# Kernel optimization log

Measured on AMD Instinct MI355X. Metric: run time of the kernel, lower is better.

The kernel has to match this reference:

```python
import jax, jax.numpy as jnp
import numpy as np

N, E, R, F, HD = 4096, 2048, 4, 128, 256
DEG_EPS = 1e-8
BN_EPS = 1e-5
LN_EPS = 1e-5


def _xavier(k, shape):
    scale = np.sqrt(2.0 / (shape[-2] + shape[-1])).astype(np.float32)
    return jax.random.normal(k, shape, jnp.float32) * scale


def setup_inputs() -> dict:
    key = jax.random.key(0)
    ks = jax.random.split(key, 8)
    X = jax.random.normal(ks[0], (N, F), jnp.float32)
    # sparse binary incidence matrices, one per relation type, stacked [R,N,E]
    H = (jax.random.uniform(ks[1], (R, N, E)) < 0.05).astype(jnp.float32)
    return {
        "X": X,
        "H": H,
        "W1": _xavier(ks[2], (R, F, HD)),
        "W2": _xavier(ks[3], (R, HD, HD)),
        "W3": _xavier(ks[4], (R, HD, F)),
        "imp": jnp.ones((3, R), jnp.float32),        # relation_importance per conv layer
        "b1": jnp.zeros((HD,), jnp.float32),
        "b2": jnp.zeros((HD,), jnp.float32),
        "b3": jnp.zeros((F,), jnp.float32),
        "bn_gamma": jnp.ones((2, HD), jnp.float32),
        "bn_beta": jnp.zeros((2, HD), jnp.float32),
        "ln_gamma": jnp.ones((2, HD), jnp.float32),
        "ln_beta": jnp.zeros((2, HD), jnp.float32),
        "rel_attn": jnp.ones((R,), jnp.float32) / R,
    }


def typed_conv(X, Hw, W, imp, bias):
    # Hw: [R,N,E] weighted incidence; theta = Dv^{-1/2} H De^{-1/2} via row/col scaling
    dv = jnp.power(Hw.sum(axis=2) + DEG_EPS, -0.5)   # [R,N]
    de = jnp.power(Hw.sum(axis=1) + DEG_EPS, -0.5)   # [R,E]
    theta = Hw * dv[:, :, None] * de[:, None, :]     # [R,N,E]
    # (theta @ theta^T) @ X computed as theta @ (theta^T @ X) -- same math, no NxN
    t = jnp.einsum('rne,nf->ref', theta, X)          # [R,E,Fin]
    Hn = jnp.einsum('rne,ref->rnf', theta, t)        # [R,N,Fin]
    out = jnp.einsum('rnf,rfo->rno', Hn, W)          # [R,N,Fout]
    out = out * jax.nn.sigmoid(imp)[:, None, None]
    return out.sum(axis=0) + bias


def bn_ln_elu(X, bg, bb, lg, lb):
    # BatchNorm1d with batch statistics (biased var), then LayerNorm, then ELU
    mu = X.mean(axis=0)
    var = X.var(axis=0)
    X = (X - mu) * jax.lax.rsqrt(var + BN_EPS) * bg + bb
    m = X.mean(axis=-1, keepdims=True)
    v = X.var(axis=-1, keepdims=True)
    X = (X - m) * jax.lax.rsqrt(v + LN_EPS) * lg + lb
    return jax.nn.elu(X)


def reference(X, H, W1, W2, W3, imp, b1, b2, b3, bn_gamma, bn_beta, ln_gamma, ln_beta, rel_attn):
    rw = jax.nn.softmax(rel_attn)
    Hw = H * rw[:, None, None]                       # weighted incidence per relation
    h = typed_conv(X, Hw, W1, imp[0], b1)
    h = bn_ln_elu(h, bn_gamma[0], bn_beta[0], ln_gamma[0], ln_beta[0])
    h = typed_conv(h, Hw, W2, imp[1], b2)
    h = bn_ln_elu(h, bn_gamma[1], bn_beta[1], ln_gamma[1], ln_beta[1])
    out = typed_conv(h, Hw, W3, imp[2], b3)
    return out + X  # residual: out_channels == in_channels by construction
```

## Files before the change

kernel.cpp:

```cpp
#include <hip/hip_runtime.h>
#include <hip/hip_bf16.h>

#define NN 4096
#define EE 2048
#define RR 4
#define FF 128
#define HDD 256

typedef __attribute__((ext_vector_type(4))) float floatx4;
typedef __attribute__((ext_vector_type(8))) __bf16 bf16x8;

#define AS1 __attribute__((address_space(1)))
#define AS3 __attribute__((address_space(3)))

__device__ __forceinline__ void async16(const void* g, void* l) {
  __builtin_amdgcn_global_load_lds((const AS1 void*)(unsigned long long)(g),
                                   (AS3 void*)(unsigned int)(unsigned long long)(l),
                                   16, 0, 0);
}

__device__ inline unsigned short f2b(float x) {
  unsigned int u = __float_as_uint(x);
  unsigned int r = u + 0x7fffu + ((u >> 16) & 1u);
  return (unsigned short)(r >> 16);
}
__device__ inline float b2f(unsigned short u) { return __uint_as_float((unsigned int)u << 16); }

__device__ inline float rel_w(const float* rel, int r) {
  float m = fmaxf(fmaxf(rel[0], rel[1]), fmaxf(rel[2], rel[3]));
  float s = 0.f;
#pragma unroll
  for (int i = 0; i < RR; i++) s += expf(rel[i] - m);
  return expf(rel[r] - m) / s;
}

__global__ void k_dvmask(const float* __restrict__ H, const float* __restrict__ rel,
                         float* __restrict__ dvs, unsigned long long* __restrict__ mask) {
  int wave = (blockIdx.x << 2) | (threadIdx.x >> 6);
  int lane = threadIdx.x & 63;
  int r = wave >> 12;
  const float* row = H + (size_t)wave * EE;
  unsigned long long* mrow = mask + (size_t)wave * (EE / 64);
  float s = 0.f;
  for (int j = 0; j < EE / 64; j++) {
    float h = row[j * 64 + lane];
    s += h;
    unsigned long long m = __ballot(h != 0.0f);
    if (lane == 0) mrow[j] = m;
  }
  for (int off = 32; off; off >>= 1) s += __shfl_down(s, off);
  if (lane == 0) {
    float rwr = rel_w(rel, r);
    dvs[wave] = rwr * rsqrtf(rwr * s + 1e-8f);
  }
}

__global__ void k_maskT(const unsigned long long* __restrict__ m1, unsigned long long* __restrict__ m2,
                        float* __restrict__ de) {
  __shared__ unsigned long long w[64 * 33];
  int r = blockIdx.x >> 6;
  int n0 = (blockIdx.x & 63) << 6;
  int t = threadIdx.x;
  const unsigned long long* src = m1 + ((size_t)r * NN + n0) * 32;
#pragma unroll
  for (int i = 0; i < 8; i++) {
    int idx = t + i * 256;
    int n = idx >> 5, W = idx & 31;
    w[n * 33 + W] = src[idx];
  }
  __syncthreads();
  int wid = t >> 6, lane = t & 63;
  int v = n0 >> 6;
#pragma unroll
  for (int Wi = 0; Wi < 8; Wi++) {
    int W = wid * 8 + Wi;
    unsigned long long myw = w[lane * 33 + W];
    unsigned long long out = 0;
    for (int b = 0; b < 64; b++) {
      unsigned long long mm = __ballot(((myw >> b) & 1ULL) != 0);
      if (lane == b) out = mm;
    }
    m2[((size_t)r * EE + W * 64 + lane) * 64 + v] = out;
    atomicAdd(&de[r * EE + W * 64 + lane], (float)__popcll(out));
  }
}

__global__ void k_deR(const float* __restrict__ de, const float* __restrict__ rel,
                      float* __restrict__ deR, float* __restrict__ deR2) {
  int i = blockIdx.x * 256 + threadIdx.x;
  int r = i >> 11;
  float rwr = rel_w(rel, r);
  float d = rsqrtf(rwr * de[i] + 1e-8f);
  deR[i] = d;
  deR2[i] = d * d;
}

__global__ void k_cvtTs(const float* __restrict__ src, const float* __restrict__ dvs,
                        unsigned short* __restrict__ dst, int M, int C) {
  __shared__ unsigned short tile[64][65];
  int r = blockIdx.z;
  int c0 = blockIdx.x * 64, m0 = blockIdx.y * 64;
  int tr = threadIdx.x >> 4, tc = threadIdx.x & 15;
#pragma unroll
  for (int i = 0; i < 4; i++) {
    int m = m0 + tr + 16 * i;
    float d = dvs[(size_t)r * M + m];
    float4 v = *(const float4*)(src + (size_t)m * C + c0 + tc * 4);
    tile[tr + 16 * i][tc * 4 + 0] = f2b(v.x * d);
    tile[tr + 16 * i][tc * 4 + 1] = f2b(v.y * d);
    tile[tr + 16 * i][tc * 4 + 2] = f2b(v.z * d);
    tile[tr + 16 * i][tc * 4 + 3] = f2b(v.w * d);
  }
  __syncthreads();
  unsigned short* db = dst + (size_t)r * C * M;
#pragma unroll
  for (int i = 0; i < 4; i++) {
    int c = c0 + tr + 16 * i;
    ushort4 v;
    v.x = tile[tc * 4 + 0][tr + 16 * i];
    v.y = tile[tc * 4 + 1][tr + 16 * i];
    v.z = tile[tc * 4 + 2][tr + 16 * i];
    v.w = tile[tc * 4 + 3][tr + 16 * i];
    *(ushort4*)(db + (size_t)c * M + m0 + tc * 4) = v;
  }
}

__global__ void k_trzs(const unsigned short* __restrict__ src, const float* __restrict__ dvs,
                       unsigned short* __restrict__ dst, int M, int C) {
  __shared__ unsigned short tile[64][65];
  int r = blockIdx.z;
  int c0 = blockIdx.x * 64, m0 = blockIdx.y * 64;
  int tr = threadIdx.x >> 4, tc = threadIdx.x & 15;
#pragma unroll
  for (int i = 0; i < 4; i++) {
    int m = m0 + tr + 16 * i;
    float d = dvs[(size_t)r * M + m];
    ushort4 v = *(const ushort4*)(src + (size_t)m * C + c0 + tc * 4);
    tile[tr + 16 * i][tc * 4 + 0] = f2b(b2f(v.x) * d);
    tile[tr + 16 * i][tc * 4 + 1] = f2b(b2f(v.y) * d);
    tile[tr + 16 * i][tc * 4 + 2] = f2b(b2f(v.z) * d);
    tile[tr + 16 * i][tc * 4 + 3] = f2b(b2f(v.w) * d);
  }
  __syncthreads();
  unsigned short* db = dst + (size_t)r * C * M;
#pragma unroll
  for (int i = 0; i < 4; i++) {
    int c = c0 + tr + 16 * i;
    ushort4 v;
    v.x = tile[tc * 4 + 0][tr + 16 * i];
    v.y = tile[tc * 4 + 1][tr + 16 * i];
    v.z = tile[tc * 4 + 2][tr + 16 * i];
    v.w = tile[tc * 4 + 3][tr + 16 * i];
    *(ushort4*)(db + (size_t)c * M + m0 + tc * 4) = v;
  }
}

__global__ void k_wprep(const float* __restrict__ W1, const float* __restrict__ W2,
                        const float* __restrict__ W3, const float* __restrict__ imp,
                        unsigned short* __restrict__ W1catT, unsigned short* __restrict__ W2T,
                        unsigned short* __restrict__ W3T) {
  int idx = blockIdx.x * 256 + threadIdx.x;
  if (idx < RR * FF * HDD) {
    int o = idx % HDD, f = (idx / HDD) % FF, r = idx / (HDD * FF);
    float sg = 1.0f / (1.0f + expf(-imp[r]));
    W1catT[(size_t)o * (RR * FF) + r * FF + f] = f2b(sg * W1[((size_t)r * FF + f) * HDD + o]);
  } else if (idx < RR * FF * HDD + RR * HDD * HDD) {
    int j = idx - RR * FF * HDD;
    int c = j % HDD, o = (j / HDD) % HDD, r = j / (HDD * HDD);
    float sg = 1.0f / (1.0f + expf(-imp[RR + r]));
    W2T[j] = f2b(sg * W2[((size_t)r * HDD + c) * HDD + o]);
  } else {
    int j = idx - RR * FF * HDD - RR * HDD * HDD;
    int c = j % HDD, o = (j / HDD) % FF, r = j / (HDD * FF);
    float sg = 1.0f / (1.0f + expf(-imp[2 * RR + r]));
    W3T[j] = f2b(sg * W3[((size_t)r * HDD + c) * FF + o]);
  }
}

template <int DECA, int DECB>
__global__ __launch_bounds__(256) void k_gemm3(
    const unsigned short* __restrict__ A, const unsigned short* __restrict__ BT,
    int K, int SK, int lda, int ldb, long a_rs, long b_rs,
    unsigned short* __restrict__ P, long c_ps, long c_rs, int ldc,
    const unsigned long long* __restrict__ dm, int dnw, long drow_rs,
    const float* __restrict__ cscale, long cs_rs) {
  __shared__ unsigned short Al[128 * 64];
  __shared__ unsigned short Bl[128 * 64];
  int tid = threadIdx.x, wid = tid >> 6, lane = tid & 63;
  int m0 = blockIdx.x << 7, n0 = blockIdx.y << 7;
  int z = blockIdx.z, zr = z / SK, kz = z - zr * SK;
  int Kc = K / SK;
  int r8 = lane >> 3, c8 = lane & 7;
  int swz = ((c8 ^ r8) << 3);
  const unsigned short* Ab = A + (DECA ? 0 : ((size_t)zr * a_rs + (size_t)m0 * lda + (size_t)kz * Kc));
  const unsigned short* Bb = BT + (DECB ? 0 : ((size_t)zr * b_rs + (size_t)n0 * ldb + (size_t)kz * Kc));
  const unsigned int* mrow = nullptr;
  int drow = 0, dhalf = 0, dsw = 0;
  unsigned short* Dl = DECA ? Al : Bl;
  if (DECA || DECB) {
    drow = tid >> 1; dhalf = tid & 1;
    long mrowOff = (long)zr * drow_rs + (DECA ? m0 : n0) + drow;
    mrow = (const unsigned int*)(dm + (size_t)mrowOff * dnw);
    dsw = drow & 7;
  }
  int wm = (wid >> 1) << 6, wn = (wid & 1) << 6;
  int fm = lane & 15, quad = lane >> 4;
  int f7 = fm & 7;
  floatx4 acc[4][4];
#pragma unroll
  for (int i = 0; i < 4; i++)
#pragma unroll
    for (int j = 0; j < 4; j++) acc[i][j] = (floatx4){0.f, 0.f, 0.f, 0.f};
  for (int k0 = 0; k0 < Kc; k0 += 64) {
    if (!DECA) {
#pragma unroll
      for (int t = 0; t < 4; t++) {
        int rbase = (wid << 5) + (t << 3);
        int row = rbase + r8;
        async16(Ab + (size_t)row * lda + k0 + swz, &Al[rbase * 64 + lane * 8]);
      }
    }
    if (!DECB) {
#pragma unroll
      for (int t = 0; t < 4; t++) {
        int rbase = (wid << 5) + (t << 3);
        int row = rbase + r8;
        async16(Bb + (size_t)row * ldb + k0 + swz, &Bl[rbase * 64 + lane * 8]);
      }
    }
    if (DECA || DECB) {
      long kglob = (long)kz * Kc + k0;
      unsigned int bits = mrow[(kglob >> 5) + dhalf];
      uint4 zz = {0u, 0u, 0u, 0u};
#pragma unroll
      for (int g = 0; g < 4; g++) {
        int chunk = ((dhalf << 2) | g) ^ dsw;
        *(uint4*)&Dl[drow * 64 + chunk * 8] = zz;
      }
      while (bits) {
        int b = __builtin_ctz(bits);
        bits &= bits - 1;
        int kl = (dhalf << 5) + b;
        Dl[drow * 64 + (((kl >> 3) ^ dsw) << 3) + (kl & 7)] = (unsigned short)0x3F80;
      }
    }
    __syncthreads();
#pragma unroll
    for (int ks = 0; ks < 2; ks++) {
      int kg = (ks << 2) | quad;
      int ko = ((kg ^ f7) << 3);
      bf16x8 a[4], b[4];
#pragma unroll
      for (int i = 0; i < 4; i++) {
        a[i] = *(const bf16x8*)&Al[(wm + i * 16 + fm) * 64 + ko];
        b[i] = *(const bf16x8*)&Bl[(wn + i * 16 + fm) * 64 + ko];
      }
#pragma unroll
      for (int i = 0; i < 4; i++)
#pragma unroll
        for (int j = 0; j < 4; j++)
          acc[i][j] = __builtin_amdgcn_mfma_f32_16x16x32_bf16(a[i], b[j], acc[i][j], 0, 0, 0);
    }
    __syncthreads();
  }
  unsigned short* Cb = P + (size_t)kz * c_ps + (size_t)zr * c_rs;
  float csc[4];
#pragma unroll
  for (int ni = 0; ni < 4; ni++)
    csc[ni] = cscale ? cscale[(size_t)zr * cs_rs + n0 + wn + ni * 16 + fm] : 1.0f;
#pragma unroll
  for (int mi = 0; mi < 4; mi++)
#pragma unroll
    for (int ni = 0; ni < 4; ni++)
#pragma unroll
      for (int v = 0; v < 4; v++) {
        int row = m0 + wm + mi * 16 + quad * 4 + v;
        int col = n0 + wn + ni * 16 + fm;
        Cb[(size_t)row * ldc + col] = f2b(acc[mi][ni][v] * csc[ni]);
      }
}

__global__ void k_red_b(const unsigned short* __restrict__ P, unsigned short* __restrict__ out,
                        int SK, long region,
                        const float* __restrict__ sc, long sc_rs, int sc_shift, int sc_mask) {
  long i = ((long)blockIdx.x * 256 + threadIdx.x) * 8;
  int zr = blockIdx.y;
  const unsigned short* p = P + (size_t)zr * SK * region + i;
  float s[8] = {0, 0, 0, 0, 0, 0, 0, 0};
  for (int k = 0; k < SK; k++) {
    const unsigned short* q = p + (size_t)k * region;
    ushort4 a = *(const ushort4*)q;
    ushort4 b = *(const ushort4*)(q + 4);
    s[0] += b2f(a.x); s[1] += b2f(a.y); s[2] += b2f(a.z); s[3] += b2f(a.w);
    s[4] += b2f(b.x); s[5] += b2f(b.y); s[6] += b2f(b.z); s[7] += b2f(b.w);
  }
  float scl[8];
#pragma unroll
  for (int j = 0; j < 8; j++)
    scl[j] = sc ? sc[(size_t)zr * sc_rs + (int)(((i + j) >> sc_shift) & sc_mask)] : 1.0f;
  ushort4 o0, o1;
  o0.x = f2b(s[0] * scl[0]); o0.y = f2b(s[1] * scl[1]); o0.z = f2b(s[2] * scl[2]); o0.w = f2b(s[3] * scl[3]);
  o1.x = f2b(s[4] * scl[4]); o1.y = f2b(s[5] * scl[5]); o1.z = f2b(s[6] * scl[6]); o1.w = f2b(s[7] * scl[7]);
  unsigned short* d = out + (size_t)zr * region + i;
  *(ushort4*)d = o0;
  *(ushort4*)(d + 4) = o1;
}

__global__ void k_red_hcatb(const unsigned short* __restrict__ P, unsigned short* __restrict__ out,
                            int SK, const float* __restrict__ dvs) {
  long i = ((long)blockIdx.x * 256 + threadIdx.x) * 8;
  int r = blockIdx.y;
  const unsigned short* p = P + (size_t)r * SK * (NN * FF) + i;
  float s[8] = {0, 0, 0, 0, 0, 0, 0, 0};
  for (int k = 0; k < SK; k++) {
    const unsigned short* q = p + (size_t)k * (NN * FF);
    ushort4 a = *(const ushort4*)q;
    ushort4 b = *(const ushort4*)(q + 4);
    s[0] += b2f(a.x); s[1] += b2f(a.y); s[2] += b2f(a.z); s[3] += b2f(a.w);
    s[4] += b2f(b.x); s[5] += b2f(b.y); s[6] += b2f(b.z); s[7] += b2f(b.w);
  }
  long n = i >> 7;
  int f = (int)(i & 127);
  float dv = dvs[(size_t)r * NN + n];
  ushort4 o0, o1;
  o0.x = f2b(s[0] * dv); o0.y = f2b(s[1] * dv); o0.z = f2b(s[2] * dv); o0.w = f2b(s[3] * dv);
  o1.x = f2b(s[4] * dv); o1.y = f2b(s[5] * dv); o1.z = f2b(s[6] * dv); o1.w = f2b(s[7] * dv);
  unsigned short* d = out + n * (RR * FF) + r * FF + f;
  *(ushort4*)d = o0;
  *(ushort4*)(d + 4) = o1;
}

__global__ void k_redstats(const unsigned short* __restrict__ P, float* __restrict__ out,
                           float* __restrict__ cs, float* __restrict__ cs2, int Z,
                           const float* __restrict__ rs, int rshift) {
  __shared__ float sm[2][8][256];
  int cg = (threadIdx.x & 31) << 3;
  int rowt = threadIdx.x >> 5;
  int r0 = blockIdx.x * 32;
  float s[8] = {0, 0, 0, 0, 0, 0, 0, 0}, s2[8] = {0, 0, 0, 0, 0, 0, 0, 0};
  for (int j = 0; j < 4; j++) {
    int row = r0 + rowt * 4 + j;
    long idx = (long)row * HDD + cg;
    float acc[8] = {0, 0, 0, 0, 0, 0, 0, 0};
    for (int z = 0; z < Z; z++) {
      const unsigned short* p = P + (size_t)z * ((long)NN * HDD) + idx;
      float w_ = rs ? rs[(size_t)(z >> rshift) * NN + row] : 1.0f;
      ushort4 a = *(const ushort4*)p;
      ushort4 b = *(const ushort4*)(p + 4);
      acc[0] += b2f(a.x) * w_; acc[1] += b2f(a.y) * w_; acc[2] += b2f(a.z) * w_; acc[3] += b2f(a.w) * w_;
      acc[4] += b2f(b.x) * w_; acc[5] += b2f(b.y) * w_; acc[6] += b2f(b.z) * w_; acc[7] += b2f(b.w) * w_;
    }
    float4 o0 = {acc[0], acc[1], acc[2], acc[3]};
    float4 o1 = {acc[4], acc[5], acc[6], acc[7]};
    *(float4*)(out + idx) = o0;
    *(float4*)(out + idx + 4) = o1;
#pragma unroll
    for (int i = 0; i < 8; i++) { s[i] += acc[i]; s2[i] += acc[i] * acc[i]; }
  }
#pragma unroll
  for (int i = 0; i < 8; i++) { sm[0][rowt][cg + i] = s[i]; sm[1][rowt][cg + i] = s2[i]; }
  __syncthreads();
  int c = threadIdx.x;
  float a0 = 0, a1 = 0;
#pragma unroll
  for (int t = 0; t < 8; t++) { a0 += sm[0][t][c]; a1 += sm[1][t][c]; }
  atomicAdd(&cs[c], a0);
  atomicAdd(&cs2[c], a1);
}

__global__ void k_red_out(const unsigned short* __restrict__ P, const float* __restrict__ X,
                          const float* __restrict__ b3, float* __restrict__ out, int Z,
                          const float* __restrict__ rs) {
  long i = ((long)blockIdx.x * 256 + threadIdx.x) * 4;
  long n = i >> 7;
  int f = (int)(i & 127);
  float4 s = *(const float4*)(X + i);
  s.x += b3[f]; s.y += b3[f + 1]; s.z += b3[f + 2]; s.w += b3[f + 3];
  for (int z = 0; z < Z; z++) {
    float w_ = rs[(size_t)(z >> 1) * NN + n];
    ushort4 v = *(const ushort4*)(P + (size_t)z * (NN * FF) + i);
    s.x += b2f(v.x) * w_; s.y += b2f(v.y) * w_; s.z += b2f(v.z) * w_; s.w += b2f(v.w) * w_;
  }
  *(float4*)(out + i) = s;
}

__global__ void k_bnlnelu(const float* __restrict__ x, const float* __restrict__ cs, const float* __restrict__ cs2,
                          const float* __restrict__ bg, const float* __restrict__ bb,
                          const float* __restrict__ lg, const float* __restrict__ lb,
                          unsigned short* __restrict__ out) {
  int wid = threadIdx.x >> 6, lane = threadIdx.x & 63;
  int n = blockIdx.x * 4 + wid;
  float y[4];
  float m = 0.f;
#pragma unroll
  for (int j = 0; j < 4; j++) {
    int c = lane + 64 * j;
    float mu = cs[c] * (1.0f / NN);
    float var = cs2[c] * (1.0f / NN) - mu * mu;
    float xv = x[(size_t)n * HDD + c];
    y[j] = (xv - mu) * rsqrtf(var + 1e-5f) * bg[c] + bb[c];
    m += y[j];
  }
  for (int off = 32; off; off >>= 1) m += __shfl_down(m, off);
  m = __shfl(m, 0) * (1.0f / HDD);
  float var = 0.f;
#pragma unroll
  for (int j = 0; j < 4; j++) { float d = y[j] - m; var += d * d; }
  for (int off = 32; off; off >>= 1) var += __shfl_down(var, off);
  var = __shfl(var, 0) * (1.0f / HDD);
  float inv = rsqrtf(var + 1e-5f);
#pragma unroll
  for (int j = 0; j < 4; j++) {
    int c = lane + 64 * j;
    float z = (y[j] - m) * inv * lg[c] + lb[c];
    z = z > 0.f ? z : expm1f(z);
    out[(size_t)n * HDD + c] = f2b(z);
  }
}

extern "C" void kernel_launch(void* const* d_in, const int* in_sizes, int n_in,
                              void* d_out, int out_size, void* d_ws, size_t ws_size,
                              hipStream_t stream) {
  const float* X   = (const float*)d_in[0];
  const float* H   = (const float*)d_in[1];
  const float* W1  = (const float*)d_in[2];
  const float* W2  = (const float*)d_in[3];
  const float* W3  = (const float*)d_in[4];
  const float* imp = (const float*)d_in[5];
  const float* b3  = (const float*)d_in[8];
  const float* bng = (const float*)d_in[9];
  const float* bnb = (const float*)d_in[10];
  const float* lng = (const float*)d_in[11];
  const float* lnb = (const float*)d_in[12];
  const float* rel = (const float*)d_in[13];
  (void)in_sizes; (void)n_in; (void)out_size; (void)ws_size;

  char* w = (char*)d_ws;
  size_t off = 0;
  auto alloc = [&](size_t bytes) -> void* {
    void* p = w + off;
    off += (bytes + 255) & ~(size_t)255;
    return p;
  };
  float* dvs  = (float*)alloc((size_t)RR * NN * 4);
  float* de   = (float*)alloc((size_t)RR * EE * 4);
  float* deR  = (float*)alloc((size_t)RR * EE * 4);
  float* deR2 = (float*)alloc((size_t)RR * EE * 4);
  float* cs   = (float*)alloc(2 * HDD * 4);
  unsigned long long* mask1 = (unsigned long long*)alloc((size_t)RR * NN * (EE / 64) * 8);
  unsigned long long* mask2 = (unsigned long long*)alloc((size_t)RR * EE * (NN / 64) * 8);
  unsigned short* bufP = (unsigned short*)alloc((size_t)16 * NN * HDD * 2);
  unsigned short* bufC = (unsigned short*)alloc((size_t)RR * EE * HDD * 2);
  unsigned short* bufD = (unsigned short*)alloc((size_t)RR * EE * HDD * 2);
  unsigned short* bufE = (unsigned short*)alloc((size_t)RR * EE * HDD * 2);
  float* convout = (float*)alloc((size_t)NN * HDD * 4);
  unsigned short* Xb   = (unsigned short*)alloc((size_t)NN * HDD * 2);
  unsigned short* XdvT = (unsigned short*)alloc((size_t)RR * FF * NN * 2);
  unsigned short* hdvT = (unsigned short*)alloc((size_t)RR * HDD * NN * 2);
  unsigned short* W1catT = (unsigned short*)alloc((size_t)RR * FF * HDD * 2);
  unsigned short* W2T    = (unsigned short*)alloc((size_t)RR * HDD * HDD * 2);
  unsigned short* W3T    = (unsigned short*)alloc((size_t)RR * HDD * FF * 2);

  k_dvmask<<<(RR * NN) / 4, 256, 0, stream>>>(H, rel, dvs, mask1);
  hipMemsetAsync(de, 0, (size_t)RR * EE * 4, stream);
  k_maskT<<<RR * (NN / 64), 256, 0, stream>>>(mask1, mask2, de);
  k_deR<<<(RR * EE) / 256, 256, 0, stream>>>(de, rel, deR, deR2);
  k_cvtTs<<<dim3(FF / 64, NN / 64, RR), 256, 0, stream>>>(X, dvs, XdvT, NN, FF);
  k_wprep<<<(RR * FF * HDD + RR * HDD * HDD + RR * HDD * FF) / 256, 256, 0, stream>>>(
      W1, W2, W3, imp, W1catT, W2T, W3T);

  k_gemm3<0, 1><<<dim3(1, EE / 128, RR * 8), 256, 0, stream>>>(
      XdvT, nullptr, NN, 8, NN, 0, (long)FF * NN, 0,
      bufP, (long)FF * EE, 8L * FF * EE, EE, mask2, NN / 64, EE, nullptr, 0);
  k_red_b<<<dim3((FF * EE) / 2048, RR), 256, 0, stream>>>(
      bufP, bufC, 8, (long)FF * EE, deR2, EE, 0, EE - 1);
  k_gemm3<1, 0><<<dim3(NN / 128, 1, RR * 2), 256, 0, stream>>>(
      nullptr, bufC, EE, 2, 0, EE, 0, (long)FF * EE,
      bufP, (long)NN * FF, 2L * NN * FF, FF, mask1, EE / 64, NN, nullptr, 0);
  k_red_hcatb<<<dim3((NN * FF) / 2048, RR), 256, 0, stream>>>(bufP, bufD, 2, dvs);
  k_gemm3<0, 0><<<dim3(NN / 128, HDD / 128, 4), 256, 0, stream>>>(
      bufD, W1catT, RR * FF, 4, RR * FF, RR * FF, 0, 0,
      bufP, (long)NN * HDD, 0, HDD, nullptr, 0, 0, nullptr, 0);
  hipMemsetAsync(cs, 0, 2 * HDD * 4, stream);
  k_redstats<<<NN / 32, 256, 0, stream>>>(bufP, convout, cs, cs + HDD, 4, nullptr, 0);
  k_bnlnelu<<<NN / 4, 256, 0, stream>>>(convout, cs, cs + HDD, bng, bnb, lng, lnb, Xb);
  k_trzs<<<dim3(HDD / 64, NN / 64, RR), 256, 0, stream>>>(Xb, dvs, hdvT, NN, HDD);

  k_gemm3<1, 0><<<dim3(EE / 128, HDD / 128, RR * 4), 256, 0, stream>>>(
      nullptr, hdvT, NN, 4, 0, NN, 0, (long)HDD * NN,
      bufP, (long)RR * EE * HDD, (long)EE * HDD, HDD, mask2, NN / 64, EE, nullptr, 0);
  k_red_b<<<dim3((RR * EE * HDD) / 2048, 1), 256, 0, stream>>>(
      bufP, bufD, 4, (long)RR * EE * HDD, deR, 0, 8, RR * EE - 1);
  k_gemm3<0, 0><<<dim3(HDD / 128, EE / 128, RR), 256, 0, stream>>>(
      W2T, bufD, HDD, 1, HDD, HDD, (long)HDD * HDD, (long)EE * HDD,
      bufE, 0, (long)HDD * EE, EE, nullptr, 0, 0, deR, EE);
  k_gemm3<1, 0><<<dim3(NN / 128, HDD / 128, RR * 2), 256, 0, stream>>>(
      nullptr, bufE, EE, 2, 0, EE, 0, (long)HDD * EE,
      bufP, (long)NN * HDD, 2L * NN * HDD, HDD, mask1, EE / 64, NN, nullptr, 0);
  hipMemsetAsync(cs, 0, 2 * HDD * 4, stream);
  k_redstats<<<NN / 32, 256, 0, stream>>>(bufP, convout, cs, cs + HDD, 8, dvs, 1);
  k_bnlnelu<<<NN / 4, 256, 0, stream>>>(convout, cs, cs + HDD, bng + HDD, bnb + HDD, lng + HDD, lnb + HDD, Xb);

  k_gemm3<0, 0><<<dim3(1, NN / 128, RR), 256, 0, stream>>>(
      W3T, Xb, HDD, 1, HDD, HDD, (long)FF * HDD, 0,
      bufD, 0, (long)FF * NN, NN, nullptr, 0, 0, dvs, NN);
  k_gemm3<0, 1><<<dim3(1, EE / 128, RR * 8), 256, 0, stream>>>(
      bufD, nullptr, NN, 8, NN, 0, (long)FF * NN, 0,
      bufP, (long)FF * EE, 8L * FF * EE, EE, mask2, NN / 64, EE, nullptr, 0);
  k_red_b<<<dim3((FF * EE) / 2048, RR), 256, 0, stream>>>(
      bufP, bufC, 8, (long)FF * EE, deR2, EE, 0, EE - 1);
  k_gemm3<1, 0><<<dim3(NN / 128, 1, RR * 2), 256, 0, stream>>>(
      nullptr, bufC, EE, 2, 0, EE, 0, (long)FF * EE,
      bufP, (long)NN * FF, 2L * NN * FF, FF, mask1, EE / 64, NN, nullptr, 0);
  k_red_out<<<(NN * FF) / 1024, 256, 0, stream>>>(bufP, X, b3, (float*)d_out, 8, dvs);
}
```

Baseline: 491.4 us.

## Fuse prep kernels, double-buffer GEMM LDS, and reorder layer-2 weight multiply

Merges the degree/mask, weight-prep and memset work into two combined prep kernels, and folds the de-scaling computation into the reduction kernel. This removes several small launches and memsets. The GEMM now double-buffers its LDS tiles so the next K-slice loads while the current one is computed. Layer 2 applies W2 before the hypergraph propagation (h·W then theta·theta^T), changing the GEMM chain and intermediate layouts. The costs are double the LDS per block, which may lower occupancy, a different bf16 rounding order in layer 2, and a K loop that assumes Kc is a multiple of 64.

```diff
diff --git a/kernel.cpp b/kernel.cpp
--- a/kernel.cpp
+++ b/kernel.cpp
@@ -34,146 +34,112 @@
   return expf(rel[r] - m) / s;
 }
 
-__global__ void k_dvmask(const float* __restrict__ H, const float* __restrict__ rel,
-                         float* __restrict__ dvs, unsigned long long* __restrict__ mask) {
-  int wave = (blockIdx.x << 2) | (threadIdx.x >> 6);
-  int lane = threadIdx.x & 63;
-  int r = wave >> 12;
-  const float* row = H + (size_t)wave * EE;
-  unsigned long long* mrow = mask + (size_t)wave * (EE / 64);
-  float s = 0.f;
-  for (int j = 0; j < EE / 64; j++) {
-    float h = row[j * 64 + lane];
-    s += h;
-    unsigned long long m = __ballot(h != 0.0f);
-    if (lane == 0) mrow[j] = m;
-  }
-  for (int off = 32; off; off >>= 1) s += __shfl_down(s, off);
-  if (lane == 0) {
-    float rwr = rel_w(rel, r);
-    dvs[wave] = rwr * rsqrtf(rwr * s + 1e-8f);
-  }
-}
-
-__global__ void k_maskT(const unsigned long long* __restrict__ m1, unsigned long long* __restrict__ m2,
-                        float* __restrict__ de) {
+__global__ void k_prep1(const float* __restrict__ H, const float* __restrict__ rel,
+                        const float* __restrict__ W1, const float* __restrict__ W2,
+                        const float* __restrict__ W3, const float* __restrict__ imp,
+                        float* __restrict__ dvs, unsigned long long* __restrict__ mask,
+                        unsigned short* __restrict__ W1catT, unsigned short* __restrict__ W2T,
+                        unsigned short* __restrict__ W3T, float* __restrict__ de, float* __restrict__ cs) {
+  int b = blockIdx.x;
+  if (b < 4096) {
+    int wave = (b << 2) | (threadIdx.x >> 6);
+    int lane = threadIdx.x & 63;
+    int r = wave >> 12;
+    const float* row = H + (size_t)wave * EE;
+    unsigned long long* mrow = mask + (size_t)wave * (EE / 64);
+    float s = 0.f;
+    for (int j = 0; j < EE / 64; j++) {
+      float h = row[j * 64 + lane];
+      s += h;
+      unsigned long long m = __ballot(h != 0.0f);
+      if (lane == 0) mrow[j] = m;
+    }
+    for (int off = 32; off; off >>= 1) s += __shfl_down(s, off);
+    if (lane == 0) {
+      float rwr = rel_w(rel, r);
+      dvs[wave] = rwr * rsqrtf(rwr * s + 1e-8f);
+    }
+  } else if (b < 4096 + 2048) {
+    int idx = (b - 4096) * 256 + threadIdx.x;
+    if (idx < RR * FF * HDD) {
+      int o = idx % HDD, f = (idx / HDD) % FF, r = idx / (HDD * FF);
+      float sg = 1.0f / (1.0f + expf(-imp[r]));
+      W1catT[(size_t)o * (RR * FF) + r * FF + f] = f2b(sg * W1[((size_t)r * FF + f) * HDD + o]);
+    } else if (idx < RR * FF * HDD + RR * HDD * HDD) {
+      int j = idx - RR * FF * HDD;
+      int c = j % HDD, o = (j / HDD) % HDD, r = j / (HDD * HDD);
+      float sg = 1.0f / (1.0f + expf(-imp[RR + r]));
+      W2T[j] = f2b(sg * W2[((size_t)r * HDD + c) * HDD + o]);
+    } else {
+      int j = idx - RR * FF * HDD - RR * HDD * HDD;
+      int c = j % HDD, o = (j / HDD) % FF, r = j / (HDD * FF);
+      float sg = 1.0f / (1.0f + expf(-imp[2 * RR + r]));
+      W3T[j] = f2b(sg * W3[((size_t)r * HDD + c) * FF + o]);
+    }
+  } else {
+    int i = (b - 6144) * 256 + threadIdx.x;
+    if (i < RR * EE) de[i] = 0.f;
+    else if (i < RR * EE + 2 * HDD) cs[i - RR * EE] = 0.f;
+  }
+}
+
+__global__ void k_prep2(const unsigned long long* __restrict__ m1, unsigned long long* __restrict__ m2,
+                        float* __restrict__ de, const float* __restrict__ X,
+                        const float* __restrict__ dvs, unsigned short* __restrict__ XdvT) {
   __shared__ unsigned long long w[64 * 33];
-  int r = blockIdx.x >> 6;
-  int n0 = (blockIdx.x & 63) << 6;
+  __shared__ unsigned short tile[64][65];
   int t = threadIdx.x;
-  const unsigned long long* src = m1 + ((size_t)r * NN + n0) * 32;
-#pragma unroll
-  for (int i = 0; i < 8; i++) {
-    int idx = t + i * 256;
-    int n = idx >> 5, W = idx & 31;
-    w[n * 33 + W] = src[idx];
-  }
-  __syncthreads();
-  int wid = t >> 6, lane = t & 63;
-  int v = n0 >> 6;
-#pragma unroll
-  for (int Wi = 0; Wi < 8; Wi++) {
-    int W = wid * 8 + Wi;
-    unsigned long long myw = w[lane * 33 + W];
-    unsigned long long out = 0;
-    for (int b = 0; b < 64; b++) {
-      unsigned long long mm = __ballot(((myw >> b) & 1ULL) != 0);
-      if (lane == b) out = mm;
-    }
-    m2[((size_t)r * EE + W * 64 + lane) * 64 + v] = out;
-    atomicAdd(&de[r * EE + W * 64 + lane], (float)__popcll(out));
-  }
-}
-
-__global__ void k_deR(const float* __restrict__ de, const float* __restrict__ rel,
-                      float* __restrict__ deR, float* __restrict__ deR2) {
-  int i = blockIdx.x * 256 + threadIdx.x;
-  int r = i >> 11;
-  float rwr = rel_w(rel, r);
-  float d = rsqrtf(rwr * de[i] + 1e-8f);
-  deR[i] = d;
-  deR2[i] = d * d;
-}
-
-__global__ void k_cvtTs(const float* __restrict__ src, const float* __restrict__ dvs,
-                        unsigned short* __restrict__ dst, int M, int C) {
-  __shared__ unsigned short tile[64][65];
-  int r = blockIdx.z;
-  int c0 = blockIdx.x * 64, m0 = blockIdx.y * 64;
-  int tr = threadIdx.x >> 4, tc = threadIdx.x & 15;
-#pragma unroll
-  for (int i = 0; i < 4; i++) {
-    int m = m0 + tr + 16 * i;
-    float d = dvs[(size_t)r * M + m];
-    float4 v = *(const float4*)(src + (size_t)m * C + c0 + tc * 4);
-    tile[tr + 16 * i][tc * 4 + 0] = f2b(v.x * d);
-    tile[tr + 16 * i][tc * 4 + 1] = f2b(v.y * d);
-    tile[tr + 16 * i][tc * 4 + 2] = f2b(v.z * d);
-    tile[tr + 16 * i][tc * 4 + 3] = f2b(v.w * d);
-  }
-  __syncthreads();
-  unsigned short* db = dst + (size_t)r * C * M;
-#pragma unroll
-  for (int i = 0; i < 4; i++) {
-    int c = c0 + tr + 16 * i;
-    ushort4 v;
-    v.x = tile[tc * 4 + 0][tr + 16 * i];
-    v.y = tile[tc * 4 + 1][tr + 16 * i];
-    v.z = tile[tc * 4 + 2][tr + 16 * i];
-    v.w = tile[tc * 4 + 3][tr + 16 * i];
-    *(ushort4*)(db + (size_t)c * M + m0 + tc * 4) = v;
-  }
-}
-
-__global__ void k_trzs(const unsigned short* __restrict__ src, const float* __restrict__ dvs,
-                       unsigned short* __restrict__ dst, int M, int C) {
-  __shared__ unsigned short tile[64][65];
-  int r = blockIdx.z;
-  int c0 = blockIdx.x * 64, m0 = blockIdx.y * 64;
-  int tr = threadIdx.x >> 4, tc = threadIdx.x & 15;
-#pragma unroll
-  for (int i = 0; i < 4; i++) {
-    int m = m0 + tr + 16 * i;
-    float d = dvs[(size_t)r * M + m];
-    ushort4 v = *(const ushort4*)(src + (size_t)m * C + c0 + tc * 4);
-    tile[tr + 16 * i][tc * 4 + 0] = f2b(b2f(v.x) * d);
-    tile[tr + 16 * i][tc * 4 + 1] = f2b(b2f(v.y) * d);
-    tile[tr + 16 * i][tc * 4 + 2] = f2b(b2f(v.z) * d);
-    tile[tr + 16 * i][tc * 4 + 3] = f2b(b2f(v.w) * d);
-  }
-  __syncthreads();
-  unsigned short* db = dst + (size_t)r * C * M;
-#pragma unroll
-  for (int i = 0; i < 4; i++) {
-    int c = c0 + tr + 16 * i;
-    ushort4 v;
-    v.x = tile[tc * 4 + 0][tr + 16 * i];
-    v.y = tile[tc * 4 + 1][tr + 16 * i];
-    v.z = tile[tc * 4 + 2][tr + 16 * i];
-    v.w = tile[tc * 4 + 3][tr + 16 * i];
-    *(ushort4*)(db + (size_t)c * M + m0 + tc * 4) = v;
-  }
-}
-
-__global__ void k_wprep(const float* __restrict__ W1, const float* __restrict__ W2,
-                        const float* __restrict__ W3, const float* __restrict__ imp,
-                        unsigned short* __restrict__ W1catT, unsigned short* __restrict__ W2T,
-                        unsigned short* __restrict__ W3T) {
-  int idx = blockIdx.x * 256 + threadIdx.x;
-  if (idx < RR * FF * HDD) {
-    int o = idx % HDD, f = (idx / HDD) % FF, r = idx / (HDD * FF);
-    float sg = 1.0f / (1.0f + expf(-imp[r]));
-    W1catT[(size_t)o * (RR * FF) + r * FF + f] = f2b(sg * W1[((size_t)r * FF + f) * HDD + o]);
-  } else if (idx < RR * FF * HDD + RR * HDD * HDD) {
-    int j = idx - RR * FF * HDD;
-    int c = j % HDD, o = (j / HDD) % HDD, r = j / (HDD * HDD);
-    float sg = 1.0f / (1.0f + expf(-imp[RR + r]));
-    W2T[j] = f2b(sg * W2[((size_t)r * HDD + c) * HDD + o]);
+  if (blockIdx.x < 256) {
+    int r = blockIdx.x >> 6;
+    int n0 = (blockIdx.x & 63) << 6;
+    const unsigned long long* src = m1 + ((size_t)r * NN + n0) * 32;
+#pragma unroll
+    for (int i = 0; i < 8; i++) {
+      int idx = t + i * 256;
+      int n = idx >> 5, W = idx & 31;
+      w[n * 33 + W] = src[idx];
+    }
+    __syncthreads();
+    int wid = t >> 6, lane = t & 63;
+    int v = n0 >> 6;
+#pragma unroll
+    for (int Wi = 0; Wi < 8; Wi++) {
+      int W = wid * 8 + Wi;
+      unsigned long long myw = w[lane * 33 + W];
+      unsigned long long out = 0;
+      for (int b = 0; b < 64; b++) {
+        unsigned long long mm = __ballot(((myw >> b) & 1ULL) != 0);
+        if (lane == b) out = mm;
+      }
+      m2[((size_t)r * EE + W * 64 + lane) * 64 + v] = out;
+      atomicAdd(&de[r * EE + W * 64 + lane], (float)__popcll(out));
+    }
   } else {
-    int j = idx - RR * FF * HDD - RR * HDD * HDD;
-    int c = j % HDD, o = (j / HDD) % FF, r = j / (HDD * FF);
-    float sg = 1.0f / (1.0f + expf(-imp[2 * RR + r]));
-    W3T[j] = f2b(sg * W3[((size_t)r * HDD + c) * FF + o]);
+    int idx = blockIdx.x - 256;
+    int c0 = (idx & 1) * 64, m0 = ((idx >> 1) & 63) * 64, r = idx >> 7;
+    int tr = t >> 4, tc = t & 15;
+#pragma unroll
+    for (int i = 0; i < 4; i++) {
+      int m = m0 + tr + 16 * i;
+      float d = dvs[(size_t)r * NN + m];
+      float4 v = *(const float4*)(X + (size_t)m * FF + c0 + tc * 4);
+      tile[tr + 16 * i][tc * 4 + 0] = f2b(v.x * d);
+      tile[tr + 16 * i][tc * 4 + 1] = f2b(v.y * d);
+      tile[tr + 16 * i][tc * 4 + 2] = f2b(v.z * d);
+      tile[tr + 16 * i][tc * 4 + 3] = f2b(v.w * d);
+    }
+    __syncthreads();
+    unsigned short* db = XdvT + (size_t)r * FF * NN;
+#pragma unroll
+    for (int i = 0; i < 4; i++) {
+      int c = c0 + tr + 16 * i;
+      ushort4 v;
+      v.x = tile[tc * 4 + 0][tr + 16 * i];
+      v.y = tile[tc * 4 + 1][tr + 16 * i];
+      v.z = tile[tc * 4 + 2][tr + 16 * i];
+      v.w = tile[tc * 4 + 3][tr + 16 * i];
+      *(ushort4*)(db + (size_t)c * NN + m0 + tc * 4) = v;
+    }
   }
 }
 
@@ -184,8 +150,8 @@
     unsigned short* __restrict__ P, long c_ps, long c_rs, int ldc,
     const unsigned long long* __restrict__ dm, int dnw, long drow_rs,
     const float* __restrict__ cscale, long cs_rs) {
-  __shared__ unsigned short Al[128 * 64];
-  __shared__ unsigned short Bl[128 * 64];
+  __shared__ unsigned short Al[2][128 * 64];
+  __shared__ unsigned short Bl[2][128 * 64];
   int tid = threadIdx.x, wid = tid >> 6, lane = tid & 63;
   int m0 = blockIdx.x << 7, n0 = blockIdx.y << 7;
   int z = blockIdx.z, zr = z / SK, kz = z - zr * SK;
@@ -196,28 +162,19 @@
   const unsigned short* Bb = BT + (DECB ? 0 : ((size_t)zr * b_rs + (size_t)n0 * ldb + (size_t)kz * Kc));
   const unsigned int* mrow = nullptr;
   int drow = 0, dhalf = 0, dsw = 0;
-  unsigned short* Dl = DECA ? Al : Bl;
   if (DECA || DECB) {
     drow = tid >> 1; dhalf = tid & 1;
     long mrowOff = (long)zr * drow_rs + (DECA ? m0 : n0) + drow;
     mrow = (const unsigned int*)(dm + (size_t)mrowOff * dnw);
     dsw = drow & 7;
   }
-  int wm = (wid >> 1) << 6, wn = (wid & 1) << 6;
-  int fm = lane & 15, quad = lane >> 4;
-  int f7 = fm & 7;
-  floatx4 acc[4][4];
-#pragma unroll
-  for (int i = 0; i < 4; i++)
-#pragma unroll
-    for (int j = 0; j < 4; j++) acc[i][j] = (floatx4){0.f, 0.f, 0.f, 0.f};
-  for (int k0 = 0; k0 < Kc; k0 += 64) {
+  auto stage = [&](int pb, int k0) {
     if (!DECA) {
 #pragma unroll
       for (int t = 0; t < 4; t++) {
         int rbase = (wid << 5) + (t << 3);
         int row = rbase + r8;
-        async16(Ab + (size_t)row * lda + k0 + swz, &Al[rbase * 64 + lane * 8]);
+        async16(Ab + (size_t)row * lda + k0 + swz, &Al[pb][rbase * 64 + lane * 8]);
       }
     }
     if (!DECB) {
@@ -225,10 +182,11 @@
       for (int t = 0; t < 4; t++) {
         int rbase = (wid << 5) + (t << 3);
         int row = rbase + r8;
-        async16(Bb + (size_t)row * ldb + k0 + swz, &Bl[rbase * 64 + lane * 8]);
+        async16(Bb + (size_t)row * ldb + k0 + swz, &Bl[pb][rbase * 64 + lane * 8]);
       }
     }
     if (DECA || DECB) {
+      unsigned short* Dl = DECA ? &Al[pb][0] : &Bl[pb][0];
       long kglob = (long)kz * Kc + k0;
       unsigned int bits = mrow[(kglob >> 5) + dhalf];
       uint4 zz = {0u, 0u, 0u, 0u};
@@ -244,7 +202,16 @@
         Dl[drow * 64 + (((kl >> 3) ^ dsw) << 3) + (kl & 7)] = (unsigned short)0x3F80;
       }
     }
-    __syncthreads();
+  };
+  int wm = (wid >> 1) << 6, wn = (wid & 1) << 6;
+  int fm = lane & 15, quad = lane >> 4;
+  int f7 = fm & 7;
+  floatx4 acc[4][4];
+#pragma unroll
+  for (int i = 0; i < 4; i++)
+#pragma unroll
+    for (int j = 0; j < 4; j++) acc[i][j] = (floatx4){0.f, 0.f, 0.f, 0.f};
+  auto compute = [&](int pb) {
 #pragma unroll
     for (int ks = 0; ks < 2; ks++) {
       int kg = (ks << 2) | quad;
@@ -252,8 +219,8 @@
       bf16x8 a[4], b[4];
 #pragma unroll
       for (int i = 0; i < 4; i++) {
-        a[i] = *(const bf16x8*)&Al[(wm + i * 16 + fm) * 64 + ko];
-        b[i] = *(const bf16x8*)&Bl[(wn + i * 16 + fm) * 64 + ko];
+        a[i] = *(const bf16x8*)&Al[pb][(wm + i * 16 + fm) * 64 + ko];
+        b[i] = *(const bf16x8*)&Bl[pb][(wn + i * 16 + fm) * 64 + ko];
       }
 #pragma unroll
       for (int i = 0; i < 4; i++)
@@ -261,6 +228,15 @@
         for (int j = 0; j < 4; j++)
           acc[i][j] = __builtin_amdgcn_mfma_f32_16x16x32_bf16(a[i], b[j], acc[i][j], 0, 0, 0);
     }
+  };
+  stage(0, 0);
+  __syncthreads();
+  for (int k0 = 0; k0 < Kc; k0 += 128) {
+    if (k0 + 64 < Kc) stage(1, k0 + 64);
+    compute(0);
+    __syncthreads();
+    if (k0 + 128 < Kc) stage(0, k0 + 128);
+    compute(1);
     __syncthreads();
   }
   unsigned short* Cb = P + (size_t)kz * c_ps + (size_t)zr * c_rs;
@@ -281,8 +257,12 @@
 }
 
 __global__ void k_red_b(const unsigned short* __restrict__ P, unsigned short* __restrict__ out,
-                        int SK, long region,
-                        const float* __restrict__ sc, long sc_rs, int sc_shift, int sc_mask) {
+                        int SK, long region, const float* __restrict__ de,
+                        const float* __restrict__ rel, float* __restrict__ cszero) {
+  if (cszero && blockIdx.x == 0 && blockIdx.y == 0) {
+    cszero[threadIdx.x] = 0.f;
+    cszero[threadIdx.x + 256] = 0.f;
+  }
   long i = ((long)blockIdx.x * 256 + threadIdx.x) * 8;
   int zr = blockIdx.y;
   const unsigned short* p = P + (size_t)zr * SK * region + i;
@@ -294,10 +274,11 @@
     s[0] += b2f(a.x); s[1] += b2f(a.y); s[2] += b2f(a.z); s[3] += b2f(a.w);
     s[4] += b2f(b.x); s[5] += b2f(b.y); s[6] += b2f(b.z); s[7] += b2f(b.w);
   }
+  float rwr = rel_w(rel, zr);
+  int e0 = (int)(i & (EE - 1));
   float scl[8];
 #pragma unroll
-  for (int j = 0; j < 8; j++)
-    scl[j] = sc ? sc[(size_t)zr * sc_rs + (int)(((i + j) >> sc_shift) & sc_mask)] : 1.0f;
+  for (int j = 0; j < 8; j++) scl[j] = 1.0f / (rwr * de[zr * EE + e0 + j] + 1e-8f);
   ushort4 o0, o1;
   o0.x = f2b(s[0] * scl[0]); o0.y = f2b(s[1] * scl[1]); o0.z = f2b(s[2] * scl[2]); o0.w = f2b(s[3] * scl[3]);
   o1.x = f2b(s[4] * scl[4]); o1.y = f2b(s[5] * scl[5]); o1.z = f2b(s[6] * scl[6]); o1.w = f2b(s[7] * scl[7]);
@@ -444,8 +425,6 @@
   };
   float* dvs  = (float*)alloc((size_t)RR * NN * 4);
   float* de   = (float*)alloc((size_t)RR * EE * 4);
-  float* deR  = (float*)alloc((size_t)RR * EE * 4);
-  float* deR2 = (float*)alloc((size_t)RR * EE * 4);
   float* cs   = (float*)alloc(2 * HDD * 4);
   unsigned long long* mask1 = (unsigned long long*)alloc((size_t)RR * NN * (EE / 64) * 8);
   unsigned long long* mask2 = (unsigned long long*)alloc((size_t)RR * EE * (NN / 64) * 8);
@@ -454,26 +433,22 @@
   unsigned short* bufD = (unsigned short*)alloc((size_t)RR * EE * HDD * 2);
   unsigned short* bufE = (unsigned short*)alloc((size_t)RR * EE * HDD * 2);
   float* convout = (float*)alloc((size_t)NN * HDD * 4);
-  unsigned short* Xb   = (unsigned short*)alloc((size_t)NN * HDD * 2);
-  unsigned short* XdvT = (unsigned short*)alloc((size_t)RR * FF * NN * 2);
-  unsigned short* hdvT = (unsigned short*)alloc((size_t)RR * HDD * NN * 2);
+  unsigned short* Xb    = (unsigned short*)alloc((size_t)NN * HDD * 2);
+  unsigned short* XdvT  = (unsigned short*)alloc((size_t)RR * FF * NN * 2);
+  unsigned short* hwdvT = (unsigned short*)alloc((size_t)RR * HDD * NN * 2);
   unsigned short* W1catT = (unsigned short*)alloc((size_t)RR * FF * HDD * 2);
   unsigned short* W2T    = (unsigned short*)alloc((size_t)RR * HDD * HDD * 2);
   unsigned short* W3T    = (unsigned short*)alloc((size_t)RR * HDD * FF * 2);
 
-  k_dvmask<<<(RR * NN) / 4, 256, 0, stream>>>(H, rel, dvs, mask1);
-  hipMemsetAsync(de, 0, (size_t)RR * EE * 4, stream);
-  k_maskT<<<RR * (NN / 64), 256, 0, stream>>>(mask1, mask2, de);
-  k_deR<<<(RR * EE) / 256, 256, 0, stream>>>(de, rel, deR, deR2);
-  k_cvtTs<<<dim3(FF / 64, NN / 64, RR), 256, 0, stream>>>(X, dvs, XdvT, NN, FF);
-  k_wprep<<<(RR * FF * HDD + RR * HDD * HDD + RR * HDD * FF) / 256, 256, 0, stream>>>(
-      W1, W2, W3, imp, W1catT, W2T, W3T);
+  k_prep1<<<4096 + 2048 + 34, 256, 0, stream>>>(H, rel, W1, W2, W3, imp,
+                                                dvs, mask1, W1catT, W2T, W3T, de, cs);
+  k_prep2<<<256 + 512, 256, 0, stream>>>(mask1, mask2, de, X, dvs, XdvT);
 
   k_gemm3<0, 1><<<dim3(1, EE / 128, RR * 8), 256, 0, stream>>>(
       XdvT, nullptr, NN, 8, NN, 0, (long)FF * NN, 0,
       bufP, (long)FF * EE, 8L * FF * EE, EE, mask2, NN / 64, EE, nullptr, 0);
   k_red_b<<<dim3((FF * EE) / 2048, RR), 256, 0, stream>>>(
-      bufP, bufC, 8, (long)FF * EE, deR2, EE, 0, EE - 1);
+      bufP, bufC, 8, (long)FF * EE, de, rel, nullptr);
   k_gemm3<1, 0><<<dim3(NN / 128, 1, RR * 2), 256, 0, stream>>>(
       nullptr, bufC, EE, 2, 0, EE, 0, (long)FF * EE,
       bufP, (long)NN * FF, 2L * NN * FF, FF, mask1, EE / 64, NN, nullptr, 0);
@@ -481,23 +456,20 @@
   k_gemm3<0, 0><<<dim3(NN / 128, HDD / 128, 4), 256, 0, stream>>>(
       bufD, W1catT, RR * FF, 4, RR * FF, RR * FF, 0, 0,
       bufP, (long)NN * HDD, 0, HDD, nullptr, 0, 0, nullptr, 0);
-  hipMemsetAsync(cs, 0, 2 * HDD * 4, stream);
   k_redstats<<<NN / 32, 256, 0, stream>>>(bufP, convout, cs, cs + HDD, 4, nullptr, 0);
   k_bnlnelu<<<NN / 4, 256, 0, stream>>>(convout, cs, cs + HDD, bng, bnb, lng, lnb, Xb);
-  k_trzs<<<dim3(HDD / 64, NN / 64, RR), 256, 0, stream>>>(Xb, dvs, hdvT, NN, HDD);
-
-  k_gemm3<1, 0><<<dim3(EE / 128, HDD / 128, RR * 4), 256, 0, stream>>>(
-      nullptr, hdvT, NN, 4, 0, NN, 0, (long)HDD * NN,
-      bufP, (long)RR * EE * HDD, (long)EE * HDD, HDD, mask2, NN / 64, EE, nullptr, 0);
-  k_red_b<<<dim3((RR * EE * HDD) / 2048, 1), 256, 0, stream>>>(
-      bufP, bufD, 4, (long)RR * EE * HDD, deR, 0, 8, RR * EE - 1);
-  k_gemm3<0, 0><<<dim3(HDD / 128, EE / 128, RR), 256, 0, stream>>>(
-      W2T, bufD, HDD, 1, HDD, HDD, (long)HDD * HDD, (long)EE * HDD,
-      bufE, 0, (long)HDD * EE, EE, nullptr, 0, 0, deR, EE);
+
+  k_gemm3<0, 0><<<dim3(HDD / 128, NN / 128, RR), 256, 0, stream>>>(
+      W2T, Xb, HDD, 1, HDD, HDD, (long)HDD * HDD, 0,
+      hwdvT, 0, (long)HDD * NN, NN, nullptr, 0, 0, dvs, NN);
+  k_gemm3<0, 1><<<dim3(HDD / 128, EE / 128, RR * 4), 256, 0, stream>>>(
+      hwdvT, nullptr, NN, 4, NN, 0, (long)HDD * NN, 0,
+      bufP, (long)HDD * EE, 4L * HDD * EE, EE, mask2, NN / 64, EE, nullptr, 0);
+  k_red_b<<<dim3((HDD * EE) / 2048, RR), 256, 0, stream>>>(
+      bufP, bufE, 4, (long)HDD * EE, de, rel, cs);
   k_gemm3<1, 0><<<dim3(NN / 128, HDD / 128, RR * 2), 256, 0, stream>>>(
       nullptr, bufE, EE, 2, 0, EE, 0, (long)HDD * EE,
       bufP, (long)NN * HDD, 2L * NN * HDD, HDD, mask1, EE / 64, NN, nullptr, 0);
-  hipMemsetAsync(cs, 0, 2 * HDD * 4, stream);
   k_redstats<<<NN / 32, 256, 0, stream>>>(bufP, convout, cs, cs + HDD, 8, dvs, 1);
   k_bnlnelu<<<NN / 4, 256, 0, stream>>>(convout, cs, cs + HDD, bng + HDD, bnb + HDD, lng + HDD, lnb + HDD, Xb);
 
@@ -508,7 +480,7 @@
       bufD, nullptr, NN, 8, NN, 0, (long)FF * NN, 0,
       bufP, (long)FF * EE, 8L * FF * EE, EE, mask2, NN / 64, EE, nullptr, 0);
   k_red_b<<<dim3((FF * EE) / 2048, RR), 256, 0, stream>>>(
-      bufP, bufC, 8, (long)FF * EE, deR2, EE, 0, EE - 1);
+      bufP, bufC, 8, (long)FF * EE, de, rel, nullptr);
   k_gemm3<1, 0><<<dim3(NN / 128, 1, RR * 2), 256, 0, stream>>>(
       nullptr, bufC, EE, 2, 0, EE, 0, (long)FF * EE,
       bufP, (long)NN * FF, 2L * NN * FF, FF, mask1, EE / 64, NN, nullptr, 0);
```

Result: faster. 470.1 us (-4.3%).
